# Optimization experiments

Hardware: AMD Instinct MI355X
Metric: run time of the kernel (lower is better)

## Reference

```python
import jax, jax.numpy as jnp
import numpy as np

N_HEAD = 16

def setup_inputs() -> dict:
    key = jax.random.key(0)
    ks = jax.random.split(key, 5)
    B, T, C = 2, 2048, 1024
    s = 1.0 / np.sqrt(C)
    return {
        "x": jax.random.normal(ks[0], (B, T, C), dtype=jnp.float32),
        "Wq": jax.random.normal(ks[1], (C, C), dtype=jnp.float32) * s,
        "Wk": jax.random.normal(ks[2], (C, C), dtype=jnp.float32) * s,
        "Wv": jax.random.normal(ks[3], (C, C), dtype=jnp.float32) * s,
        "Wo": jax.random.normal(ks[4], (C, C), dtype=jnp.float32) * s,
        "bo": jnp.zeros((C,), dtype=jnp.float32),
    }

def reference(x, Wq, Wk, Wv, Wo, bo):
    B, T, C = x.shape
    H = N_HEAD
    D = C // H

    def shape(t):  # (B,T,C) -> (B,H,T,D)
        return t.reshape(B, T, H, D).transpose(0, 2, 1, 3)

    q = shape(x @ Wq)
    k = shape(x @ Wk)
    v = shape(x @ Wv)

    # scores: (B,H,T,Tk), Tk == T (no past_kv)
    att = jnp.einsum("bhtd,bhsd->bhts", q, k) * (1.0 / np.sqrt(D))
    i = jnp.arange(T)[:, None]
    j = jnp.arange(T)[None, :]
    causal = (j <= i)  # (T, Tk)
    att = jnp.where(causal[None, None], att, -jnp.inf)
    att = jax.nn.softmax(att, axis=-1)  # dropout=0.0 -> identity

    out = jnp.einsum("bhts,bhsd->bhtd", att, v)
    out = out.transpose(0, 2, 1, 3).reshape(B, T, C)
    out = out @ Wo + bo
    return out, (k, v)
```

## Files before the change

kernel.cpp:

```cpp
#include <hip/hip_runtime.h>
#include <hip/hip_bf16.h>

constexpr int B_ = 2;
constexpr int T_ = 2048;
constexpr int C_ = 1024;
constexpr int H_ = 16;
constexpr int D_ = 64;
constexpr int M_ = B_ * T_;

typedef __attribute__((ext_vector_type(8))) short bf16x8;
typedef __attribute__((ext_vector_type(4))) float f32x4;
typedef const __attribute__((address_space(1))) void gaddr_t;
typedef __attribute__((address_space(3))) void laddr_t;

__device__ __forceinline__ unsigned short f2bf(float f) {
    unsigned u = __float_as_uint(f);
    return (unsigned short)((u + 0x7fffu + ((u >> 16) & 1u)) >> 16);
}

union BF8 { bf16x8 v; __hip_bfloat162 h[4]; };

__device__ __forceinline__ bf16x8 cvt8(const float4 a, const float4 b) {
    BF8 r;
    r.h[0] = __float22bfloat162_rn(make_float2(a.x, a.y));
    r.h[1] = __float22bfloat162_rn(make_float2(a.z, a.w));
    r.h[2] = __float22bfloat162_rn(make_float2(b.x, b.y));
    r.h[3] = __float22bfloat162_rn(make_float2(b.z, b.w));
    return r.v;
}

__global__ __launch_bounds__(256)
void prep(const float* __restrict__ x, const float* __restrict__ Wq,
          const float* __restrict__ Wk, const float* __restrict__ Wv,
          const float* __restrict__ Wo, unsigned short* __restrict__ xb,
          unsigned short* __restrict__ wtb)
{
    const int z = blockIdx.z;
    const int tid = threadIdx.x;

    if (z == 4) {
        const int base = (blockIdx.y * 16 + blockIdx.x) * 4096 + tid;
#pragma unroll
        for (int i = 0; i < 16; ++i) {
            const int idx = base + i * 256;
            float4 v = ((const float4*)x)[idx];
            union { __hip_bfloat162 h[2]; ushort4 u; } o;
            o.h[0] = __float22bfloat162_rn(make_float2(v.x, v.y));
            o.h[1] = __float22bfloat162_rn(make_float2(v.z, v.w));
            ((ushort4*)xb)[idx] = o.u;
        }
        return;
    }

    __shared__ float tile[64][65];
    const float* W = (z == 0) ? Wq : (z == 1) ? Wk : (z == 2) ? Wv : Wo;
    unsigned short* O = wtb + (size_t)z * C_ * C_;

    const int n0 = blockIdx.x * 64, k0 = blockIdx.y * 64;
    const int r = tid >> 4, c4 = (tid & 15) * 4;

#pragma unroll
    for (int i = 0; i < 4; ++i) {
        const int kk = i * 16 + r;
        float4 v = *(const float4*)(W + (size_t)(k0 + kk) * C_ + n0 + c4);
        tile[c4 + 0][kk] = v.x;
        tile[c4 + 1][kk] = v.y;
        tile[c4 + 2][kk] = v.z;
        tile[c4 + 3][kk] = v.w;
    }
    __syncthreads();
#pragma unroll
    for (int i = 0; i < 4; ++i) {
        const int nn = i * 16 + r;
        ushort4 o;
        o.x = f2bf(tile[nn][c4 + 0]);
        o.y = f2bf(tile[nn][c4 + 1]);
        o.z = f2bf(tile[nn][c4 + 2]);
        o.w = f2bf(tile[nn][c4 + 3]);
        *(ushort4*)(O + (size_t)(n0 + nn) * C_ + k0 + c4) = o;
    }
}

template<int WRITE_KB>
__global__ __launch_bounds__(512)
void gemm_qkv(const unsigned short* __restrict__ xb, const unsigned short* __restrict__ wtb,
              unsigned short* __restrict__ qb, float* __restrict__ kout,
              float* __restrict__ vout, unsigned short* __restrict__ kb,
              unsigned short* __restrict__ vtt)
{
    __shared__ unsigned short As[3][128 * 64];
    __shared__ unsigned short Bs[3][128 * 64];

    const int tid = threadIdx.x;
    const int which = blockIdx.x >> 3;
    const int n0 = (blockIdx.x & 7) * 128;
    const int m0 = blockIdx.y * 128;
    const unsigned short* wt = wtb + (size_t)which * C_ * C_;

    const int lane = tid & 63, w = tid >> 6;
    const int wm = (w >> 2) * 64, wn2 = (w & 3) * 32;
    const int fr = lane & 15, qd = lane >> 4;

    int crow[2], cofs[2]; size_t clds[2];
#pragma unroll
    for (int cc = 0; cc < 2; ++cc) {
        const int c = tid + cc * 512;
        crow[cc] = c >> 3;
        cofs[cc] = ((c & 7) ^ (crow[cc] & 7)) * 8;
        clds[cc] = (size_t)c * 16;
    }

#define STAGE(s, kt)                                                               \
    {                                                                              \
        _Pragma("unroll")                                                          \
        for (int cc = 0; cc < 2; ++cc) {                                           \
            __builtin_amdgcn_global_load_lds(                                      \
                (gaddr_t*)(xb + (size_t)(m0 + crow[cc]) * C_ + (kt) * 64 + cofs[cc]), \
                (laddr_t*)((char*)As[s] + clds[cc]), 16, 0, 0);                    \
            __builtin_amdgcn_global_load_lds(                                      \
                (gaddr_t*)(wt + (size_t)(n0 + crow[cc]) * C_ + (kt) * 64 + cofs[cc]), \
                (laddr_t*)((char*)Bs[s] + clds[cc]), 16, 0, 0);                    \
        }                                                                          \
    }

    f32x4 acc[4][2] = {};
    constexpr int NT = C_ / 64;

    STAGE(0, 0);
    STAGE(1, 1);
    asm volatile("s_waitcnt vmcnt(4)" ::: "memory");
    __builtin_amdgcn_s_barrier();
    __builtin_amdgcn_sched_barrier(0);

    for (int t = 0; t < NT; ++t) {
        const int s = t % 3;
        if (t + 2 < NT) STAGE((t + 2) % 3, t + 2);

        const unsigned short* Ac = As[s];
        const unsigned short* Bc = Bs[s];
#pragma unroll
        for (int half = 0; half < 2; ++half) {
            bf16x8 af[4], bfv[2];
#pragma unroll
            for (int mt = 0; mt < 4; ++mt) {
                const int row = wm + mt * 16 + fr, dg = half * 4 + qd;
                af[mt] = *(const bf16x8*)&Ac[row * 64 + ((dg ^ (row & 7)) * 8)];
            }
#pragma unroll
            for (int nt = 0; nt < 2; ++nt) {
                const int row = wn2 + nt * 16 + fr, dg = half * 4 + qd;
                bfv[nt] = *(const bf16x8*)&Bc[row * 64 + ((dg ^ (row & 7)) * 8)];
            }
#pragma unroll
            for (int mt = 0; mt < 4; ++mt)
#pragma unroll
                for (int nt = 0; nt < 2; ++nt)
                    acc[mt][nt] = __builtin_amdgcn_mfma_f32_16x16x32_bf16(
                        bfv[nt], af[mt], acc[mt][nt], 0, 0, 0);
        }

        if (t + 2 < NT)      asm volatile("s_waitcnt vmcnt(4)" ::: "memory");
        else if (t + 1 < NT) asm volatile("s_waitcnt vmcnt(0)" ::: "memory");
        __builtin_amdgcn_s_barrier();
        __builtin_amdgcn_sched_barrier(0);
    }
#undef STAGE

#pragma unroll
    for (int mt = 0; mt < 4; ++mt) {
        const int mm = m0 + wm + mt * 16 + fr;
        const int b = mm >> 11, t = mm & (T_ - 1);
#pragma unroll
        for (int nt = 0; nt < 2; ++nt) {
            const int nn = n0 + wn2 + nt * 16 + qd * 4;
            const int h = nn >> 6, d0 = nn & 63;
            const int bh = b * H_ + h;
            const size_t off = ((size_t)bh * T_ + t) * D_ + d0;
            const f32x4 a4 = acc[mt][nt];
            if (which == 0) {
                *(ushort4*)(qb + off) =
                    make_ushort4(f2bf(a4[0]), f2bf(a4[1]), f2bf(a4[2]), f2bf(a4[3]));
            } else if (which == 1) {
                *(float4*)(kout + off) = make_float4(a4[0], a4[1], a4[2], a4[3]);
                if (WRITE_KB)
                    *(ushort4*)(kb + off) =
                        make_ushort4(f2bf(a4[0]), f2bf(a4[1]), f2bf(a4[2]), f2bf(a4[3]));
            } else {
                *(float4*)(vout + off) = make_float4(a4[0], a4[1], a4[2], a4[3]);
                unsigned short* vb = vtt
                    + (((size_t)bh * (T_ / 64) + (t >> 6)) * 64 + d0) * 64 + (t & 63);
#pragma unroll
                for (int r = 0; r < 4; ++r) vb[(size_t)r * 64] = f2bf(a4[r]);
            }
        }
    }
}

__global__ __launch_bounds__(512)
void gemm_o(const unsigned short* __restrict__ ab, const unsigned short* __restrict__ wot,
            const float* __restrict__ bo, float* __restrict__ out)
{
    __shared__ unsigned short As[3][128 * 64];
    __shared__ unsigned short Bs[3][128 * 64];

    const int tid = threadIdx.x;
    const int n0 = blockIdx.x * 128;
    const int m0 = blockIdx.y * 128;

    const int lane = tid & 63, w = tid >> 6;
    const int wm = (w >> 2) * 64, wn2 = (w & 3) * 32;
    const int fr = lane & 15, qd = lane >> 4;

    int crow[2], cofs[2]; size_t clds[2];
#pragma unroll
    for (int cc = 0; cc < 2; ++cc) {
        const int c = tid + cc * 512;
        crow[cc] = c >> 3;
        cofs[cc] = ((c & 7) ^ (crow[cc] & 7)) * 8;
        clds[cc] = (size_t)c * 16;
    }

#define STAGE_O(s, kt)                                                             \
    {                                                                              \
        _Pragma("unroll")                                                          \
        for (int cc = 0; cc < 2; ++cc) {                                           \
            __builtin_amdgcn_global_load_lds(                                      \
                (gaddr_t*)(ab + (size_t)(m0 + crow[cc]) * C_ + (kt) * 64 + cofs[cc]),  \
                (laddr_t*)((char*)As[s] + clds[cc]), 16, 0, 0);                    \
            __builtin_amdgcn_global_load_lds(                                      \
                (gaddr_t*)(wot + (size_t)(n0 + crow[cc]) * C_ + (kt) * 64 + cofs[cc]), \
                (laddr_t*)((char*)Bs[s] + clds[cc]), 16, 0, 0);                    \
        }                                                                          \
    }

    f32x4 acc[4][2] = {};
    constexpr int NT = C_ / 64;

    STAGE_O(0, 0);
    STAGE_O(1, 1);
    asm volatile("s_waitcnt vmcnt(4)" ::: "memory");
    __builtin_amdgcn_s_barrier();
    __builtin_amdgcn_sched_barrier(0);

    for (int t = 0; t < NT; ++t) {
        const int s = t % 3;
        if (t + 2 < NT) STAGE_O((t + 2) % 3, t + 2);

        const unsigned short* Ac = As[s];
        const unsigned short* Bc = Bs[s];
#pragma unroll
        for (int half = 0; half < 2; ++half) {
            bf16x8 af[4], bfv[2];
#pragma unroll
            for (int mt = 0; mt < 4; ++mt) {
                const int row = wm + mt * 16 + fr, dg = half * 4 + qd;
                af[mt] = *(const bf16x8*)&Ac[row * 64 + ((dg ^ (row & 7)) * 8)];
            }
#pragma unroll
            for (int nt = 0; nt < 2; ++nt) {
                const int row = wn2 + nt * 16 + fr, dg = half * 4 + qd;
                bfv[nt] = *(const bf16x8*)&Bc[row * 64 + ((dg ^ (row & 7)) * 8)];
            }
#pragma unroll
            for (int mt = 0; mt < 4; ++mt)
#pragma unroll
                for (int nt = 0; nt < 2; ++nt)
                    acc[mt][nt] = __builtin_amdgcn_mfma_f32_16x16x32_bf16(
                        bfv[nt], af[mt], acc[mt][nt], 0, 0, 0);
        }

        if (t + 2 < NT)      asm volatile("s_waitcnt vmcnt(4)" ::: "memory");
        else if (t + 1 < NT) asm volatile("s_waitcnt vmcnt(0)" ::: "memory");
        __builtin_amdgcn_s_barrier();
        __builtin_amdgcn_sched_barrier(0);
    }
#undef STAGE_O

#pragma unroll
    for (int mt = 0; mt < 4; ++mt) {
        const int mm = m0 + wm + mt * 16 + fr;
#pragma unroll
        for (int nt = 0; nt < 2; ++nt) {
            const int nn = n0 + wn2 + nt * 16 + qd * 4;
            const float4 b4 = *(const float4*)(bo + nn);
            *(float4*)(out + (size_t)mm * C_ + nn) =
                make_float4(acc[mt][nt][0] + b4.x, acc[mt][nt][1] + b4.y,
                            acc[mt][nt][2] + b4.z, acc[mt][nt][3] + b4.w);
        }
    }
}

__global__ __launch_bounds__(256)
void attn_lds(const unsigned short* __restrict__ qb, const unsigned short* __restrict__ kb,
              const unsigned short* __restrict__ vtt, unsigned short* __restrict__ attb)
{
    __shared__ unsigned short Ks[2][64 * 64];
    __shared__ unsigned short Vs[2][64 * 64];
    __shared__ alignas(16) unsigned short Pt[4][16 * 72];

    const int tid = threadIdx.x;
    const int lane = tid & 63, w = tid >> 6;
    const int fr = lane & 15, qd = lane >> 4;

    const int blk = blockIdx.x;
    const int xcd = blk & 7, within = blk >> 3;
    const int bh = xcd * 4 + (within & 3);
    const int jj = within >> 2;
    const int kk_ = jj >> 3, ii_ = jj & 7;
    const int qt = (kk_ == 0) ? (31 - ii_) : (kk_ == 1) ? ii_
                 : (kk_ == 2) ? (23 - ii_) : (8 + ii_);
    const int b = bh >> 4, h = bh & 15;

    unsigned short* Pw = Pt[w];
    const unsigned short* qB = qb  + (size_t)bh * T_ * D_;
    const unsigned short* kB = kb  + (size_t)bh * T_ * D_;
    const unsigned short* vT = vtt + (size_t)bh * (T_ / 64) * 64 * 64;

    const int qr0 = qt * 64 + w * 16;
    const int qrow_g = qr0 + fr;

    bf16x8 aq0 = *(const bf16x8*)(qB + (size_t)(qr0 + fr) * D_ + qd * 8);
    bf16x8 aq1 = *(const bf16x8*)(qB + (size_t)(qr0 + fr) * D_ + 32 + qd * 8);

    f32x4 accT[4] = {};
    float l_i = 0.0f;
    const float sc2 = 0.18033688f;

    const int L0 = w * 128 + lane, L1 = L0 + 64;
    const int r0 = L0 >> 3, e0 = (((L0 & 7) ^ (r0 & 7)) * 8);
    const int r1 = L1 >> 3, e1 = (((L1 & 7) ^ (r1 & 7)) * 8);

    {
        __builtin_amdgcn_global_load_lds((gaddr_t*)(kB + r0 * 64 + e0),
            (laddr_t*)((char*)Ks[0] + (size_t)L0 * 16), 16, 0, 0);
        __builtin_amdgcn_global_load_lds((gaddr_t*)(kB + r1 * 64 + e1),
            (laddr_t*)((char*)Ks[0] + (size_t)L1 * 16), 16, 0, 0);
        __builtin_amdgcn_global_load_lds((gaddr_t*)(vT + r0 * 64 + e0),
            (laddr_t*)((char*)Vs[0] + (size_t)L0 * 16), 16, 0, 0);
        __builtin_amdgcn_global_load_lds((gaddr_t*)(vT + r1 * 64 + e1),
            (laddr_t*)((char*)Vs[0] + (size_t)L1 * 16), 16, 0, 0);
    }
    asm volatile("s_waitcnt vmcnt(0)" ::: "memory");
    __builtin_amdgcn_s_barrier();
    __builtin_amdgcn_sched_barrier(0);

    for (int jt = 0; jt <= qt; ++jt) {
        const int cur = jt & 1;
        if (jt < qt) {
            const unsigned short* kt = kB + (size_t)((jt + 1) * 64) * 64;
            const unsigned short* vt = vT + (size_t)(jt + 1) * 4096;
            char* Kn = (char*)Ks[cur ^ 1];
            char* Vn = (char*)Vs[cur ^ 1];
            __builtin_amdgcn_global_load_lds((gaddr_t*)(kt + r0 * 64 + e0),
                (laddr_t*)(Kn + (size_t)L0 * 16), 16, 0, 0);
            __builtin_amdgcn_global_load_lds((gaddr_t*)(kt + r1 * 64 + e1),
                (laddr_t*)(Kn + (size_t)L1 * 16), 16, 0, 0);
            __builtin_amdgcn_global_load_lds((gaddr_t*)(vt + r0 * 64 + e0),
                (laddr_t*)(Vn + (size_t)L0 * 16), 16, 0, 0);
            __builtin_amdgcn_global_load_lds((gaddr_t*)(vt + r1 * 64 + e1),
                (laddr_t*)(Vn + (size_t)L1 * 16), 16, 0, 0);
        }
        const unsigned short* Kc = Ks[cur];
        const unsigned short* Vc = Vs[cur];

        bf16x8 bk[8];
#pragma unroll
        for (int q8 = 0; q8 < 8; ++q8) {
            const int row = (q8 >> 1) * 16 + fr;
            const int dg = (q8 & 1) * 4 + qd;
            bk[q8] = *(const bf16x8*)&Kc[row * 64 + ((dg ^ (row & 7)) * 8)];
        }

        f32x4 s4[4] = {};
        __builtin_amdgcn_s_setprio(1);
#pragma unroll
        for (int nt = 0; nt < 4; ++nt) {
            s4[nt] = __builtin_amdgcn_mfma_f32_16x16x32_bf16(bk[nt * 2 + 0], aq0, s4[nt], 0, 0, 0);
            s4[nt] = __builtin_amdgcn_mfma_f32_16x16x32_bf16(bk[nt * 2 + 1], aq1, s4[nt], 0, 0, 0);
        }
        __builtin_amdgcn_s_setprio(0);

        if (jt == qt) {
            const int kbase = jt * 64 + qd * 4;
#pragma unroll
            for (int nt = 0; nt < 4; ++nt)
#pragma unroll
            for (int r = 0; r < 4; ++r) {
                const int kcol = kbase + nt * 16 + r;
                const float pv = (kcol <= qrow_g)
                               ? __builtin_amdgcn_exp2f(s4[nt][r] * sc2) : 0.0f;
                s4[nt][r] = pv;
                l_i += pv;
            }
        } else {
#pragma unroll
            for (int nt = 0; nt < 4; ++nt)
#pragma unroll
            for (int r = 0; r < 4; ++r) {
                const float pv = __builtin_amdgcn_exp2f(s4[nt][r] * sc2);
                s4[nt][r] = pv;
                l_i += pv;
            }
        }

#pragma unroll
        for (int nt = 0; nt < 4; ++nt) {
            union { __hip_bfloat162 h2[2]; unsigned long long u; } pk;
            pk.h2[0] = __float22bfloat162_rn(make_float2(s4[nt][0], s4[nt][1]));
            pk.h2[1] = __float22bfloat162_rn(make_float2(s4[nt][2], s4[nt][3]));
            *(unsigned long long*)&Pw[fr * 72 + nt * 16 + qd * 4] = pk.u;
        }
        const bf16x8 ap0 = *(const bf16x8*)&Pw[fr * 72 + qd * 8];
        const bf16x8 ap1 = *(const bf16x8*)&Pw[fr * 72 + 32 + qd * 8];

        bf16x8 bv[8];
#pragma unroll
        for (int q8 = 0; q8 < 8; ++q8) {
            const int row = (q8 >> 1) * 16 + fr;
            const int dg = (q8 & 1) * 4 + qd;
            bv[q8] = *(const bf16x8*)&Vc[row * 64 + ((dg ^ (row & 7)) * 8)];
        }

        __builtin_amdgcn_s_setprio(1);
#pragma unroll
        for (int nt = 0; nt < 4; ++nt) {
            accT[nt] = __builtin_amdgcn_mfma_f32_16x16x32_bf16(bv[nt * 2 + 0], ap0, accT[nt], 0, 0, 0);
            accT[nt] = __builtin_amdgcn_mfma_f32_16x16x32_bf16(bv[nt * 2 + 1], ap1, accT[nt], 0, 0, 0);
        }
        __builtin_amdgcn_s_setprio(0);

        asm volatile("s_waitcnt vmcnt(0)" ::: "memory");
        __builtin_amdgcn_s_barrier();
        __builtin_amdgcn_sched_barrier(0);
    }

    l_i += __shfl_xor(l_i, 16);
    l_i += __shfl_xor(l_i, 32);
    const float inv = 1.0f / l_i;

#pragma unroll
    for (int nt = 0; nt < 4; ++nt) {
        union { __hip_bfloat162 h2[2]; unsigned long long u; } ok;
        ok.h2[0] = __float22bfloat162_rn(make_float2(accT[nt][0] * inv, accT[nt][1] * inv));
        ok.h2[1] = __float22bfloat162_rn(make_float2(accT[nt][2] * inv, accT[nt][3] * inv));
        *(unsigned long long*)&Pw[fr * 72 + nt * 16 + qd * 4] = ok.u;
    }
    {
        const int row = lane >> 2, d0 = (lane & 3) * 16;
        const bf16x8 o0 = *(const bf16x8*)&Pw[row * 72 + d0];
        const bf16x8 o1 = *(const bf16x8*)&Pw[row * 72 + d0 + 8];
        unsigned short* op = attb + ((size_t)b * T_ + qr0 + row) * C_ + h * 64 + d0;
        *(bf16x8*)op = o0;
        *(bf16x8*)(op + 8) = o1;
    }
}

__global__ __launch_bounds__(256)
void attn_v4(const unsigned short* __restrict__ qb, const float* __restrict__ kf,
             const unsigned short* __restrict__ vtt, unsigned short* __restrict__ attb)
{
    __shared__ alignas(16) unsigned short Pt[4][16 * 72];

    const int tid = threadIdx.x;
    const int lane = tid & 63, w = tid >> 6;
    const int fr = lane & 15, qd = lane >> 4;

    const int blk = blockIdx.x;
    const int xcd = blk & 7, within = blk >> 3;
    const int bh = xcd * 4 + (within & 3);
    const int jj = within >> 2;
    const int kk_ = jj >> 3, ii_ = jj & 7;
    const int qt = (kk_ == 0) ? (31 - ii_) : (kk_ == 1) ? ii_
                 : (kk_ == 2) ? (23 - ii_) : (8 + ii_);
    const int b = bh >> 4, h = bh & 15;

    unsigned short* Pw = Pt[w];
    const unsigned short* qB = qb  + (size_t)bh * T_ * D_;
    const float*          kB = kf  + (size_t)bh * T_ * D_;
    const unsigned short* vT = vtt + (size_t)bh * (T_ / 64) * 64 * 64;

    const int qr0 = qt * 64 + w * 16;
    const int qrow_g = qr0 + fr;

    bf16x8 aq0 = *(const bf16x8*)(qB + (size_t)(qr0 + fr) * D_ + qd * 8);
    bf16x8 aq1 = *(const bf16x8*)(qB + (size_t)(qr0 + fr) * D_ + 32 + qd * 8);

    f32x4 accT[4] = {};
    float l_i = 0.0f;
    const float sc2 = 0.18033688f;

    for (int jt = 0; jt <= qt; ++jt) {
        bf16x8 bk[8];
#pragma unroll
        for (int q8 = 0; q8 < 8; ++q8) {
            const float* p = kB + (size_t)(jt * 64 + (q8 >> 1) * 16 + fr) * D_
                           + (q8 & 1) * 32 + qd * 8;
            bk[q8] = cvt8(*(const float4*)p, *(const float4*)(p + 4));
        }
        f32x4 s4[4] = {};
#pragma unroll
        for (int nt = 0; nt < 4; ++nt) {
            s4[nt] = __builtin_amdgcn_mfma_f32_16x16x32_bf16(bk[nt * 2 + 0], aq0, s4[nt], 0, 0, 0);
            s4[nt] = __builtin_amdgcn_mfma_f32_16x16x32_bf16(bk[nt * 2 + 1], aq1, s4[nt], 0, 0, 0);
        }
        if (jt == qt) {
            const int kbase = jt * 64 + qd * 4;
#pragma unroll
            for (int nt = 0; nt < 4; ++nt)
#pragma unroll
            for (int r = 0; r < 4; ++r) {
                const int kcol = kbase + nt * 16 + r;
                const float pv = (kcol <= qrow_g)
                               ? __builtin_amdgcn_exp2f(s4[nt][r] * sc2) : 0.0f;
                s4[nt][r] = pv; l_i += pv;
            }
        } else {
#pragma unroll
            for (int nt = 0; nt < 4; ++nt)
#pragma unroll
            for (int r = 0; r < 4; ++r) {
                const float pv = __builtin_amdgcn_exp2f(s4[nt][r] * sc2);
                s4[nt][r] = pv; l_i += pv;
            }
        }
#pragma unroll
        for (int nt = 0; nt < 4; ++nt) {
            union { __hip_bfloat162 h2[2]; unsigned long long u; } pk;
            pk.h2[0] = __float22bfloat162_rn(make_float2(s4[nt][0], s4[nt][1]));
            pk.h2[1] = __float22bfloat162_rn(make_float2(s4[nt][2], s4[nt][3]));
            *(unsigned long long*)&Pw[fr * 72 + nt * 16 + qd * 4] = pk.u;
        }
        const bf16x8 ap0 = *(const bf16x8*)&Pw[fr * 72 + qd * 8];
        const bf16x8 ap1 = *(const bf16x8*)&Pw[fr * 72 + 32 + qd * 8];

        bf16x8 bv[8];
#pragma unroll
        for (int q8 = 0; q8 < 8; ++q8)
            bv[q8] = *(const bf16x8*)(vT + (size_t)jt * 4096
                                      + ((q8 >> 1) * 16 + fr) * 64 + (q8 & 1) * 32 + qd * 8);
#pragma unroll
        for (int nt = 0; nt < 4; ++nt) {
            accT[nt] = __builtin_amdgcn_mfma_f32_16x16x32_bf16(bv[nt * 2 + 0], ap0, accT[nt], 0, 0, 0);
            accT[nt] = __builtin_amdgcn_mfma_f32_16x16x32_bf16(bv[nt * 2 + 1], ap1, accT[nt], 0, 0, 0);
        }
    }

    l_i += __shfl_xor(l_i, 16);
    l_i += __shfl_xor(l_i, 32);
    const float inv = 1.0f / l_i;
#pragma unroll
    for (int nt = 0; nt < 4; ++nt) {
        union { __hip_bfloat162 h2[2]; unsigned long long u; } ok;
        ok.h2[0] = __float22bfloat162_rn(make_float2(accT[nt][0] * inv, accT[nt][1] * inv));
        ok.h2[1] = __float22bfloat162_rn(make_float2(accT[nt][2] * inv, accT[nt][3] * inv));
        *(unsigned long long*)&Pw[fr * 72 + nt * 16 + qd * 4] = ok.u;
    }
    {
        const int row = lane >> 2, d0 = (lane & 3) * 16;
        const bf16x8 o0 = *(const bf16x8*)&Pw[row * 72 + d0];
        const bf16x8 o1 = *(const bf16x8*)&Pw[row * 72 + d0 + 8];
        unsigned short* op = attb + ((size_t)b * T_ + qr0 + row) * C_ + h * 64 + d0;
        *(bf16x8*)op = o0;
        *(bf16x8*)(op + 8) = o1;
    }
}

extern "C" void kernel_launch(void* const* d_in, const int* in_sizes, int n_in,
                              void* d_out, int out_size, void* d_ws, size_t ws_size,
                              hipStream_t stream)
{
    (void)in_sizes; (void)n_in; (void)out_size;
    const float* x  = (const float*)d_in[0];
    const float* Wq = (const float*)d_in[1];
    const float* Wk = (const float*)d_in[2];
    const float* Wv = (const float*)d_in[3];
    const float* Wo = (const float*)d_in[4];
    const float* bo = (const float*)d_in[5];

    float* out  = (float*)d_out;
    float* kout = out  + (size_t)M_ * C_;
    float* vout = kout + (size_t)B_ * H_ * T_ * D_;

    unsigned short* xb   = (unsigned short*)d_ws;
    unsigned short* wtb  = xb  + (size_t)M_ * C_;
    unsigned short* qb   = wtb + (size_t)4 * C_ * C_;
    unsigned short* vtt  = qb  + (size_t)M_ * C_;
    unsigned short* kb   = vtt + (size_t)M_ * C_;
    unsigned short* attb = xb;
    const bool use_kb = ws_size >= (size_t)40 * 1024 * 1024;

    prep<<<dim3(16, 16, 5), 256, 0, stream>>>(x, Wq, Wk, Wv, Wo, xb, wtb);

    if (use_kb)
        gemm_qkv<1><<<dim3(24, 32), 512, 0, stream>>>(xb, wtb, qb, kout, vout, kb, vtt);
    else
        gemm_qkv<0><<<dim3(24, 32), 512, 0, stream>>>(xb, wtb, qb, kout, vout, kb, vtt);

    if (use_kb)
        attn_lds<<<1024, 256, 0, stream>>>(qb, kb, vtt, attb);
    else
        attn_v4<<<1024, 256, 0, stream>>>(qb, kout, vtt, attb);

    gemm_o<<<dim3(8, 32), 512, 0, stream>>>(attb, wtb + (size_t)3 * C_ * C_, bo, out);
}
```

Measured before the change: 187.2 us.

## Use 128-row query tiles with 8 waves and triple-buffered K/V staging

The attention kernel now runs 512 threads per block, each block covering 128 query rows with eight waves, so every K/V tile staged in LDS is reused by twice as many queries. The grid halves to 512 blocks and the causal tile ordering is adjusted for 16 query tiles per head. K/V staging moves from double to triple buffering with a prefetch distance of two and partial vmcnt waits, to hide global-load latency better. In exchange each block uses more LDS, there are fewer blocks to balance the causal load, and diagonal masking now applies to two tiles per block.

```diff
diff --git a/kernel.cpp b/kernel.cpp
--- a/kernel.cpp
+++ b/kernel.cpp
@@ -290,13 +290,13 @@
     }
 }
 
-__global__ __launch_bounds__(256)
+__global__ __launch_bounds__(512)
 void attn_lds(const unsigned short* __restrict__ qb, const unsigned short* __restrict__ kb,
               const unsigned short* __restrict__ vtt, unsigned short* __restrict__ attb)
 {
-    __shared__ unsigned short Ks[2][64 * 64];
-    __shared__ unsigned short Vs[2][64 * 64];
-    __shared__ alignas(16) unsigned short Pt[4][16 * 72];
+    __shared__ unsigned short Ks[3][64 * 64];
+    __shared__ unsigned short Vs[3][64 * 64];
+    __shared__ alignas(16) unsigned short Pt[8][16 * 72];
 
     const int tid = threadIdx.x;
     const int lane = tid & 63, w = tid >> 6;
@@ -306,9 +306,7 @@
     const int xcd = blk & 7, within = blk >> 3;
     const int bh = xcd * 4 + (within & 3);
     const int jj = within >> 2;
-    const int kk_ = jj >> 3, ii_ = jj & 7;
-    const int qt = (kk_ == 0) ? (31 - ii_) : (kk_ == 1) ? ii_
-                 : (kk_ == 2) ? (23 - ii_) : (8 + ii_);
+    const int qt = (jj >> 3) == 0 ? (15 - (jj & 7)) : (jj & 7);
     const int b = bh >> 4, h = bh & 15;
 
     unsigned short* Pw = Pt[w];
@@ -316,8 +314,10 @@
     const unsigned short* kB = kb  + (size_t)bh * T_ * D_;
     const unsigned short* vT = vtt + (size_t)bh * (T_ / 64) * 64 * 64;
 
-    const int qr0 = qt * 64 + w * 16;
+    const int qr0 = qt * 128 + w * 16;
     const int qrow_g = qr0 + fr;
+    const int jtmax = 2 * qt + 1;
+    const int jt_diag = qr0 >> 6;
 
     bf16x8 aq0 = *(const bf16x8*)(qB + (size_t)(qr0 + fr) * D_ + qd * 8);
     bf16x8 aq1 = *(const bf16x8*)(qB + (size_t)(qr0 + fr) * D_ + 32 + qd * 8);
@@ -326,42 +326,31 @@
     float l_i = 0.0f;
     const float sc2 = 0.18033688f;
 
-    const int L0 = w * 128 + lane, L1 = L0 + 64;
+    const int L0 = tid;
     const int r0 = L0 >> 3, e0 = (((L0 & 7) ^ (r0 & 7)) * 8);
-    const int r1 = L1 >> 3, e1 = (((L1 & 7) ^ (r1 & 7)) * 8);
-
-    {
-        __builtin_amdgcn_global_load_lds((gaddr_t*)(kB + r0 * 64 + e0),
-            (laddr_t*)((char*)Ks[0] + (size_t)L0 * 16), 16, 0, 0);
-        __builtin_amdgcn_global_load_lds((gaddr_t*)(kB + r1 * 64 + e1),
-            (laddr_t*)((char*)Ks[0] + (size_t)L1 * 16), 16, 0, 0);
-        __builtin_amdgcn_global_load_lds((gaddr_t*)(vT + r0 * 64 + e0),
-            (laddr_t*)((char*)Vs[0] + (size_t)L0 * 16), 16, 0, 0);
-        __builtin_amdgcn_global_load_lds((gaddr_t*)(vT + r1 * 64 + e1),
-            (laddr_t*)((char*)Vs[0] + (size_t)L1 * 16), 16, 0, 0);
-    }
-    asm volatile("s_waitcnt vmcnt(0)" ::: "memory");
+
+#define STAGE_KV(s, jt)                                                            \
+    {                                                                              \
+        __builtin_amdgcn_global_load_lds(                                          \
+            (gaddr_t*)(kB + (size_t)(jt) * 4096 + r0 * 64 + e0),                   \
+            (laddr_t*)((char*)Ks[s] + (size_t)L0 * 16), 16, 0, 0);                 \
+        __builtin_amdgcn_global_load_lds(                                          \
+            (gaddr_t*)(vT + (size_t)(jt) * 4096 + r0 * 64 + e0),                   \
+            (laddr_t*)((char*)Vs[s] + (size_t)L0 * 16), 16, 0, 0);                 \
+    }
+
+    STAGE_KV(0, 0);
+    STAGE_KV(1, 1);
+    asm volatile("s_waitcnt vmcnt(2)" ::: "memory");
     __builtin_amdgcn_s_barrier();
     __builtin_amdgcn_sched_barrier(0);
 
-    for (int jt = 0; jt <= qt; ++jt) {
-        const int cur = jt & 1;
-        if (jt < qt) {
-            const unsigned short* kt = kB + (size_t)((jt + 1) * 64) * 64;
-            const unsigned short* vt = vT + (size_t)(jt + 1) * 4096;
-            char* Kn = (char*)Ks[cur ^ 1];
-            char* Vn = (char*)Vs[cur ^ 1];
-            __builtin_amdgcn_global_load_lds((gaddr_t*)(kt + r0 * 64 + e0),
-                (laddr_t*)(Kn + (size_t)L0 * 16), 16, 0, 0);
-            __builtin_amdgcn_global_load_lds((gaddr_t*)(kt + r1 * 64 + e1),
-                (laddr_t*)(Kn + (size_t)L1 * 16), 16, 0, 0);
-            __builtin_amdgcn_global_load_lds((gaddr_t*)(vt + r0 * 64 + e0),
-                (laddr_t*)(Vn + (size_t)L0 * 16), 16, 0, 0);
-            __builtin_amdgcn_global_load_lds((gaddr_t*)(vt + r1 * 64 + e1),
-                (laddr_t*)(Vn + (size_t)L1 * 16), 16, 0, 0);
-        }
-        const unsigned short* Kc = Ks[cur];
-        const unsigned short* Vc = Vs[cur];
+    for (int jt = 0; jt <= jtmax; ++jt) {
+        const int s = jt % 3;
+        if (jt + 2 <= jtmax) STAGE_KV((jt + 2) % 3, jt + 2);
+
+        const unsigned short* Kc = Ks[s];
+        const unsigned short* Vc = Vs[s];
 
         bf16x8 bk[8];
 #pragma unroll
@@ -380,7 +369,7 @@
         }
         __builtin_amdgcn_s_setprio(0);
 
-        if (jt == qt) {
+        if (jt >= jt_diag) {
             const int kbase = jt * 64 + qd * 4;
 #pragma unroll
             for (int nt = 0; nt < 4; ++nt)
@@ -429,10 +418,12 @@
         }
         __builtin_amdgcn_s_setprio(0);
 
-        asm volatile("s_waitcnt vmcnt(0)" ::: "memory");
+        if (jt + 2 <= jtmax)      asm volatile("s_waitcnt vmcnt(2)" ::: "memory");
+        else if (jt + 1 <= jtmax) asm volatile("s_waitcnt vmcnt(0)" ::: "memory");
         __builtin_amdgcn_s_barrier();
         __builtin_amdgcn_sched_barrier(0);
     }
+#undef STAGE_KV
 
     l_i += __shfl_xor(l_i, 16);
     l_i += __shfl_xor(l_i, 32);
@@ -597,7 +588,7 @@
         gemm_qkv<0><<<dim3(24, 32), 512, 0, stream>>>(xb, wtb, qb, kout, vout, kb, vtt);
 
     if (use_kb)
-        attn_lds<<<1024, 256, 0, stream>>>(qb, kb, vtt, attb);
+        attn_lds<<<512, 512, 0, stream>>>(qb, kb, vtt, attb);
     else
         attn_v4<<<1024, 256, 0, stream>>>(qb, kout, vtt, attb);
 
```

After: 189.1 us. No clear change (+1.0%).
